# Kernel optimization log

Measured on AMD Instinct MI355X. Metric: run time of the kernel, lower is better.

Reference implementation:

```python
import jax, jax.numpy as jnp
import numpy as np

N_NODES = 100000
N_EDGES = 3200000
IN_CH = 128
HID = 64
N_GRAPHS = 512


def _gcn_conv(x, W, b, src, dst, n_nodes):
    """PyG GCNConv: out = D^{-1/2} (A + I) D^{-1/2} X W + b.
    src/dst are edge endpoints; self-loops handled analytically."""
    h = x @ W  # [N, out]
    # degree with self-loops (count at target nodes, as in PyG)
    deg = jnp.zeros((n_nodes,), h.dtype).at[dst].add(1.0) + 1.0
    dis = jax.lax.rsqrt(deg)  # deg^{-1/2}
    norm = dis[src] * dis[dst]  # [E]
    msg = h[src] * norm[:, None]  # gather + scale, [E, out]
    out = jnp.zeros_like(h).at[dst].add(msg)  # scatter-add
    # self-loop term: norm_ii = 1/deg_i
    out = out + h * (dis * dis)[:, None]
    return out + b


def setup_inputs() -> dict:
    key = jax.random.key(0)
    ks = jax.random.split(key, 8)
    x = jax.random.normal(ks[0], (N_NODES, IN_CH), dtype=jnp.float32)
    edge_index = jax.random.randint(ks[1], (2, N_EDGES), 0, N_NODES, dtype=jnp.int64)
    batch = jnp.sort(jax.random.randint(ks[2], (N_NODES,), 0, N_GRAPHS, dtype=jnp.int64))
    s1 = 1.0 / np.sqrt(IN_CH)
    s2 = 1.0 / np.sqrt(HID)
    W1 = jax.random.uniform(ks[3], (IN_CH, HID), jnp.float32, -s1, s1)
    b1 = jax.random.uniform(ks[4], (HID,), jnp.float32, -s1, s1)
    W2 = jax.random.uniform(ks[5], (HID, HID), jnp.float32, -s2, s2)
    b2 = jax.random.uniform(ks[6], (HID,), jnp.float32, -s2, s2)
    return {"x": x, "edge_index": edge_index, "batch": batch,
            "W1": W1, "b1": b1, "W2": W2, "b2": b2}


def reference(x, edge_index, batch, W1, b1, W2, b2):
    src, dst = edge_index[0], edge_index[1]
    n = x.shape[0]
    h = jax.nn.relu(_gcn_conv(x, W1, b1, src, dst, n))
    h = jax.nn.relu(_gcn_conv(h, W2, b2, src, dst, n))
    # F.dropout(p=0.2) treated as identity (eval / deterministic reference)
    # global_mean_pool: segment mean over graph ids
    sums = jax.ops.segment_sum(h, batch, num_segments=N_GRAPHS)
    cnts = jax.ops.segment_sum(jnp.ones((n,), h.dtype), batch, num_segments=N_GRAPHS)
    return sums / jnp.maximum(cnts, 1.0)[:, None]
```

## Files before the change

kernel.cpp:

```cpp
#include <hip/hip_runtime.h>

typedef unsigned int uint;
typedef unsigned short ushort;
typedef float f32x2 __attribute__((ext_vector_type(2)));

#define N_NODES 100000
#define N_EDGES 3200000
#define IN_CH 128
#define HID 64
#define N_GRAPHS 512
#define EPB 4096
#define NBLK ((N_EDGES + EPB - 1) / EPB)
#define NB 391
#define CAP 10240

__device__ __forceinline__ uint f2bf1(float f) {
    union { float f; uint i; } v; v.f = f;
    return (v.i + 0x7fffu + ((v.i >> 16) & 1u)) >> 16;
}
__device__ __forceinline__ uint pack2(float lo, float hi) {
    return f2bf1(lo) | (f2bf1(hi) << 16);
}
__device__ __forceinline__ float2 ub2(uint u) {
    union { uint i; float f; } a, b;
    a.i = u << 16; b.i = u & 0xffff0000u;
    return make_float2(a.f, b.f);
}
__device__ __forceinline__ f32x2 up2(uint u) {
    union { uint i; float f; } lo, hi;
    lo.i = u << 16; hi.i = u & 0xffff0000u;
    f32x2 r; r.x = lo.f; r.y = hi.f;
    return r;
}

__global__ __launch_bounds__(256) void scatter_kernel(const int* __restrict__ src,
                                                      const int* __restrict__ dst,
                                                      int* __restrict__ bcnt,
                                                      uint* __restrict__ pairs) {
    __shared__ int h4[4 * NB];
    __shared__ int gbase[NB];
    __shared__ int cur[NB];
    __shared__ int scan[512];
    __shared__ uint stage[EPB];
    __shared__ ushort sbid[EPB];
    int t = threadIdx.x;
    int base = blockIdx.x * EPB;

    int rs[16], rd[16];
#pragma unroll
    for (int j = 0; j < 16; ++j) {
        int e = base + j * 256 + t;
        if (e < N_EDGES) { rs[j] = src[e]; rd[j] = dst[e]; }
        else rd[j] = -1;
    }
    for (int i = t; i < 4 * NB; i += 256) h4[i] = 0;
    __syncthreads();
    int w = t >> 6;
#pragma unroll
    for (int j = 0; j < 16; ++j)
        if (rd[j] >= 0) atomicAdd(&h4[w * NB + (rd[j] >> 8)], 1);
    __syncthreads();

    for (int b = t; b < 512; b += 256)
        scan[b] = (b < NB) ? (h4[b] + h4[NB + b] + h4[2 * NB + b] + h4[3 * NB + b]) : 0;
    __syncthreads();
#pragma unroll
    for (int o = 1; o < 512; o <<= 1) {
        int a0 = (t >= o) ? scan[t - o] : 0;
        int a1 = (t + 256 >= o) ? scan[t + 256 - o] : 0;
        __syncthreads();
        scan[t] += a0;
        scan[t + 256] += a1;
        __syncthreads();
    }

    for (int b = t; b < NB; b += 256) {
        int cnt = h4[b] + h4[NB + b] + h4[2 * NB + b] + h4[3 * NB + b];
        int loff = scan[b] - cnt;
        int start = cnt ? atomicAdd(&bcnt[b * 16], cnt) : 0;
        gbase[b] = b * CAP + start - loff;
        cur[b] = loff;
    }
    __syncthreads();

#pragma unroll
    for (int j = 0; j < 16; ++j) {
        if (rd[j] >= 0) {
            int b = rd[j] >> 8;
            int r = atomicAdd(&cur[b], 1);
            stage[r] = ((uint)(rd[j] & 255) << 24) | (uint)rs[j];
            sbid[r] = (ushort)b;
        }
    }
    __syncthreads();

    int total = scan[NB - 1];
    for (int i = t; i < total; i += 256)
        pairs[(size_t)gbase[sbid[i]] + i] = stage[i];
}

__global__ __launch_bounds__(512) void bucket_csr_kernel(const uint* __restrict__ pairs,
                                                         const int* __restrict__ bcnt,
                                                         int* __restrict__ csr_src,
                                                         int* __restrict__ rstart,
                                                         int* __restrict__ rend,
                                                         float* __restrict__ dis) {
    __shared__ int h8[8 * 256];
    __shared__ int h[256];
    int b = blockIdx.x;
    int t = threadIdx.x;
    int w = t >> 6;
    int e0 = b * CAP;
    int e1 = e0 + bcnt[b * 16];

    for (int i = t; i < 8 * 256; i += 512) h8[i] = 0;
    __syncthreads();

    int* hw = &h8[w * 256];
    int e = e0 + t;
    for (; e + 1536 < e1; e += 2048) {
        uint p0 = pairs[e], p1 = pairs[e + 512], p2 = pairs[e + 1024], p3 = pairs[e + 1536];
        atomicAdd(&hw[p0 >> 24], 1);
        atomicAdd(&hw[p1 >> 24], 1);
        atomicAdd(&hw[p2 >> 24], 1);
        atomicAdd(&hw[p3 >> 24], 1);
    }
    for (; e < e1; e += 512)
        atomicAdd(&hw[pairs[e] >> 24], 1);
    __syncthreads();

    int v = 0;
    if (t < 256) {
#pragma unroll
        for (int j = 0; j < 8; ++j) v += h8[j * 256 + t];
        h[t] = v;
    }
    __syncthreads();
#pragma unroll
    for (int o = 1; o < 256; o <<= 1) {
        int x = (t >= o && t < 256) ? h[t - o] : 0;
        __syncthreads();
        if (t < 256) h[t] += x;
        __syncthreads();
    }
    int excl = (t < 256) ? h[t] - v : 0;
    int n = b * 256 + t;
    if (t < 256 && n < N_NODES) {
        rstart[n] = e0 + excl;
        rend[n] = e0 + excl + v;
        dis[n] = rsqrtf((float)v + 1.0f);
    }
    __syncthreads();
    if (t < 256) h[t] = e0 + excl;
    __syncthreads();

    e = e0 + t;
    for (; e + 1536 < e1; e += 2048) {
        uint p0 = pairs[e], p1 = pairs[e + 512], p2 = pairs[e + 1024], p3 = pairs[e + 1536];
        int q0 = atomicAdd(&h[p0 >> 24], 1);
        int q1 = atomicAdd(&h[p1 >> 24], 1);
        int q2 = atomicAdd(&h[p2 >> 24], 1);
        int q3 = atomicAdd(&h[p3 >> 24], 1);
        csr_src[q0] = (int)(p0 & 0xFFFFFFu);
        csr_src[q1] = (int)(p1 & 0xFFFFFFu);
        csr_src[q2] = (int)(p2 & 0xFFFFFFu);
        csr_src[q3] = (int)(p3 & 0xFFFFFFu);
    }
    for (; e < e1; e += 512) {
        uint p = pairs[e];
        int pos = atomicAdd(&h[p >> 24], 1);
        csr_src[pos] = (int)(p & 0xFFFFFFu);
    }
}

__global__ __launch_bounds__(256) void gemm1_kernel(const float* __restrict__ X,
                                                    const float* __restrict__ W,
                                                    const float* __restrict__ dis,
                                                    uint* __restrict__ Y) {
    __shared__ float Wl[IN_CH * 64];
    __shared__ float Xs[128 * 33];
    int t = threadIdx.x;
    for (int idx = t; idx < IN_CH * 64; idx += 256) Wl[idx] = W[idx];

    int r0 = (t >> 3) * 4;
    int c0 = (t & 7) * 8;
    int rowBase = blockIdx.x * 128;

    float acc[4][8];
#pragma unroll
    for (int a = 0; a < 4; ++a)
#pragma unroll
        for (int c = 0; c < 8; ++c) acc[a][c] = 0.f;

    int srow = t >> 1;
    int shh = (t & 1) * 16;
    bool sok = (rowBase + srow) < N_NODES;
    const float* xbase = X + (size_t)(rowBase + srow) * IN_CH + shh;

    float4 nx[4];
#pragma unroll
    for (int f = 0; f < 4; ++f)
        nx[f] = sok ? *reinterpret_cast<const float4*>(xbase + f * 4)
                    : make_float4(0.f, 0.f, 0.f, 0.f);

    for (int kc = 0; kc < IN_CH; kc += 32) {
        if (kc) __syncthreads();
#pragma unroll
        for (int f = 0; f < 4; ++f) {
            int o = srow * 33 + shh + f * 4;
            Xs[o] = nx[f].x; Xs[o + 1] = nx[f].y; Xs[o + 2] = nx[f].z; Xs[o + 3] = nx[f].w;
        }
        __syncthreads();
        if (kc + 32 < IN_CH) {
#pragma unroll
            for (int f = 0; f < 4; ++f)
                nx[f] = sok ? *reinterpret_cast<const float4*>(xbase + kc + 32 + f * 4)
                            : make_float4(0.f, 0.f, 0.f, 0.f);
        }
#pragma unroll
        for (int kk = 0; kk < 32; ++kk) {
            const float4 wa = *reinterpret_cast<const float4*>(&Wl[(kc + kk) * 64 + c0]);
            const float4 wb = *reinterpret_cast<const float4*>(&Wl[(kc + kk) * 64 + c0 + 4]);
            float xr[4];
#pragma unroll
            for (int a = 0; a < 4; ++a) xr[a] = Xs[(r0 + a) * 33 + kk];
#pragma unroll
            for (int a = 0; a < 4; ++a) {
                acc[a][0] += xr[a] * wa.x; acc[a][1] += xr[a] * wa.y;
                acc[a][2] += xr[a] * wa.z; acc[a][3] += xr[a] * wa.w;
                acc[a][4] += xr[a] * wb.x; acc[a][5] += xr[a] * wb.y;
                acc[a][6] += xr[a] * wb.z; acc[a][7] += xr[a] * wb.w;
            }
        }
    }
#pragma unroll
    for (int a = 0; a < 4; ++a) {
        int row = rowBase + r0 + a;
        if (row < N_NODES) {
            float d = dis[row];
            uint4 o;
            o.x = pack2(acc[a][0] * d, acc[a][1] * d);
            o.y = pack2(acc[a][2] * d, acc[a][3] * d);
            o.z = pack2(acc[a][4] * d, acc[a][5] * d);
            o.w = pack2(acc[a][6] * d, acc[a][7] * d);
            *reinterpret_cast<uint4*>(Y + (size_t)row * 32 + (t & 7) * 4) = o;
        }
    }
}

__global__ __launch_bounds__(256) void gemm2_kernel(const uint* __restrict__ X,
                                                    const float* __restrict__ W,
                                                    const float* __restrict__ dis,
                                                    uint* __restrict__ Y) {
    __shared__ float Wl[HID * 64];
    __shared__ float Xs[128 * 33];
    int t = threadIdx.x;
    for (int idx = t; idx < HID * 64; idx += 256) Wl[idx] = W[idx];

    int r0 = (t >> 3) * 4;
    int c0 = (t & 7) * 8;
    int rowBase = blockIdx.x * 128;

    float acc[4][8];
#pragma unroll
    for (int a = 0; a < 4; ++a)
#pragma unroll
        for (int c = 0; c < 8; ++c) acc[a][c] = 0.f;

    int srow = t >> 1;
    int shh = (t & 1) * 16;
    bool sok = (rowBase + srow) < N_NODES;
    const uint* xbase = X + (size_t)(rowBase + srow) * 32 + (t & 1) * 8;

    uint4 n0_ = make_uint4(0, 0, 0, 0), n1_ = n0_;
    if (sok) {
        n0_ = *reinterpret_cast<const uint4*>(xbase);
        n1_ = *reinterpret_cast<const uint4*>(xbase + 4);
    }

    for (int kc = 0; kc < HID; kc += 32) {
        if (kc) __syncthreads();
        {
            uint us[8] = {n0_.x, n0_.y, n0_.z, n0_.w, n1_.x, n1_.y, n1_.z, n1_.w};
            int o = srow * 33 + shh;
#pragma unroll
            for (int j = 0; j < 8; ++j) {
                float2 f = ub2(us[j]);
                Xs[o + 2 * j]     = fmaxf(f.x, 0.f);
                Xs[o + 2 * j + 1] = fmaxf(f.y, 0.f);
            }
        }
        __syncthreads();
        if (kc + 32 < HID && sok) {
            n0_ = *reinterpret_cast<const uint4*>(xbase + 16);
            n1_ = *reinterpret_cast<const uint4*>(xbase + 20);
        }
#pragma unroll
        for (int kk = 0; kk < 32; ++kk) {
            const float4 wa = *reinterpret_cast<const float4*>(&Wl[(kc + kk) * 64 + c0]);
            const float4 wb = *reinterpret_cast<const float4*>(&Wl[(kc + kk) * 64 + c0 + 4]);
            float xr[4];
#pragma unroll
            for (int a = 0; a < 4; ++a) xr[a] = Xs[(r0 + a) * 33 + kk];
#pragma unroll
            for (int a = 0; a < 4; ++a) {
                acc[a][0] += xr[a] * wa.x; acc[a][1] += xr[a] * wa.y;
                acc[a][2] += xr[a] * wa.z; acc[a][3] += xr[a] * wa.w;
                acc[a][4] += xr[a] * wb.x; acc[a][5] += xr[a] * wb.y;
                acc[a][6] += xr[a] * wb.z; acc[a][7] += xr[a] * wb.w;
            }
        }
    }
#pragma unroll
    for (int a = 0; a < 4; ++a) {
        int row = rowBase + r0 + a;
        if (row < N_NODES) {
            float d = dis[row];
            uint4 o;
            o.x = pack2(acc[a][0] * d, acc[a][1] * d);
            o.y = pack2(acc[a][2] * d, acc[a][3] * d);
            o.z = pack2(acc[a][4] * d, acc[a][5] * d);
            o.w = pack2(acc[a][6] * d, acc[a][7] * d);
            *reinterpret_cast<uint4*>(Y + (size_t)row * 32 + (t & 7) * 4) = o;
        }
    }
}

__global__ __launch_bounds__(256) void gather_kernel(const int* __restrict__ rstart,
                                                     const int* __restrict__ rend,
                                                     const int* __restrict__ csr_src,
                                                     const float* __restrict__ dis,
                                                     const float* __restrict__ bias,
                                                     const uint* __restrict__ A,
                                                     uint* __restrict__ B) {
    int i = blockIdx.x * 4 + (threadIdx.x >> 6);
    if (i >= N_NODES) return;
    int lane = threadIdx.x & 63;
    int q = lane >> 3;
    int cu = (lane & 7) * 4;

    float4 bi0 = *reinterpret_cast<const float4*>(&bias[(lane & 7) * 8]);
    float4 bi1 = *reinterpret_cast<const float4*>(&bias[(lane & 7) * 8 + 4]);

    int e = rstart[i];
    int end = rend[i];

    f32x2 a[4], b[4];
#pragma unroll
    for (int j = 0; j < 4; ++j) { a[j] = (f32x2)0.f; b[j] = (f32x2)0.f; }

    if (q == 0) {
        uint4 u = *reinterpret_cast<const uint4*>(&A[(size_t)i * 32 + cu]);
        a[0] += up2(u.x); a[1] += up2(u.y); a[2] += up2(u.z); a[3] += up2(u.w);
    }
    for (; e + 16 <= end; e += 16) {
        int s0 = csr_src[e + q];
        int s1 = csr_src[e + 8 + q];
        uint4 u0 = *reinterpret_cast<const uint4*>(&A[(size_t)s0 * 32 + cu]);
        uint4 u1 = *reinterpret_cast<const uint4*>(&A[(size_t)s1 * 32 + cu]);
        a[0] += up2(u0.x); a[1] += up2(u0.y); a[2] += up2(u0.z); a[3] += up2(u0.w);
        b[0] += up2(u1.x); b[1] += up2(u1.y); b[2] += up2(u1.z); b[3] += up2(u1.w);
    }
    for (; e + 8 <= end; e += 8) {
        int s = csr_src[e + q];
        uint4 u = *reinterpret_cast<const uint4*>(&A[(size_t)s * 32 + cu]);
        a[0] += up2(u.x); a[1] += up2(u.y); a[2] += up2(u.z); a[3] += up2(u.w);
    }
    if (e + q < end) {
        int s = csr_src[e + q];
        uint4 u = *reinterpret_cast<const uint4*>(&A[(size_t)s * 32 + cu]);
        b[0] += up2(u.x); b[1] += up2(u.y); b[2] += up2(u.z); b[3] += up2(u.w);
    }
    float r[8];
#pragma unroll
    for (int j = 0; j < 4; ++j) {
        f32x2 s = a[j] + b[j];
        r[2 * j] = s.x; r[2 * j + 1] = s.y;
    }
#pragma unroll
    for (int j = 0; j < 8; ++j) {
        r[j] += __shfl_xor(r[j], 8);
        r[j] += __shfl_xor(r[j], 16);
        r[j] += __shfl_xor(r[j], 32);
    }
    if (q == 0) {
        float d = dis[i];
        uint4 o;
        o.x = pack2(bi0.x + d * r[0], bi0.y + d * r[1]);
        o.y = pack2(bi0.z + d * r[2], bi0.w + d * r[3]);
        o.z = pack2(bi1.x + d * r[4], bi1.y + d * r[5]);
        o.w = pack2(bi1.z + d * r[6], bi1.w + d * r[7]);
        *reinterpret_cast<uint4*>(B + (size_t)i * 32 + (lane & 7) * 4) = o;
    }
}

__global__ __launch_bounds__(256) void pool_kernel(const uint* __restrict__ B,
                                                   const int* __restrict__ batch,
                                                   float* __restrict__ sums,
                                                   float* __restrict__ cnt) {
    int w = blockIdx.x * 4 + (threadIdx.x >> 6);
    int half = (threadIdx.x >> 5) & 1;
    int l = threadIdx.x & 31;
    int n0 = w * 32 + half * 16;
    if (n0 >= N_NODES) return;
    int n1 = min(n0 + 16, N_NODES);
    int curg = batch[n0];
    float a0 = 0.f, a1 = 0.f;
    int run = 0;
    for (int n = n0; n < n1; ++n) {
        int g = batch[n];
        if (g != curg) {
            atomicAdd(&sums[curg * 64 + 2 * l], a0);
            atomicAdd(&sums[curg * 64 + 2 * l + 1], a1);
            if (l == 0) atomicAdd(&cnt[curg], (float)run);
            curg = g; a0 = 0.f; a1 = 0.f; run = 0;
        }
        float2 f = ub2(B[(size_t)n * 32 + l]);
        a0 += fmaxf(f.x, 0.f);
        a1 += fmaxf(f.y, 0.f);
        run++;
    }
    atomicAdd(&sums[curg * 64 + 2 * l], a0);
    atomicAdd(&sums[curg * 64 + 2 * l + 1], a1);
    if (l == 0) atomicAdd(&cnt[curg], (float)run);
}

__global__ __launch_bounds__(256) void final_kernel(const float* __restrict__ sums,
                                                    const float* __restrict__ cnt,
                                                    float* __restrict__ out) {
    int idx = blockIdx.x * 256 + threadIdx.x;
    if (idx < N_GRAPHS * 64) out[idx] = sums[idx] / fmaxf(cnt[idx >> 6], 1.0f);
}

extern "C" void kernel_launch(void* const* d_in, const int* in_sizes, int n_in,
                              void* d_out, int out_size, void* d_ws, size_t ws_size,
                              hipStream_t stream) {
    const float* x     = (const float*)d_in[0];
    const int*   edge  = (const int*)d_in[1];
    const int*   batch = (const int*)d_in[2];
    const float* W1    = (const float*)d_in[3];
    const float* b1    = (const float*)d_in[4];
    const float* W2    = (const float*)d_in[5];
    const float* b2    = (const float*)d_in[6];
    float* out = (float*)d_out;

    uint*  A        = (uint*)d_ws;
    uint*  B        = A + (size_t)N_NODES * 32;
    uint*  pairs    = B + (size_t)N_NODES * 32;
    int*   csr_src  = (int*)(pairs + (size_t)NB * CAP);
    float* dis      = (float*)(csr_src + (size_t)NB * CAP);
    int*   rstart   = (int*)(dis + N_NODES);
    int*   rend     = rstart + N_NODES;
    float* sums     = (float*)(rend + N_NODES);
    float* cnt_f    = sums + (size_t)N_GRAPHS * 64;
    int*   bcnt     = (int*)(cnt_f + N_GRAPHS);

    const int* src = edge;
    const int* dst = edge + N_EDGES;

    hipMemsetAsync(sums, 0, (N_GRAPHS * 64 + N_GRAPHS + NB * 16) * sizeof(float), stream);

    scatter_kernel<<<NBLK, 256, 0, stream>>>(src, dst, bcnt, pairs);
    bucket_csr_kernel<<<NB, 512, 0, stream>>>(pairs, bcnt, csr_src, rstart, rend, dis);

    gemm1_kernel<<<(N_NODES + 127) / 128, 256, 0, stream>>>(x, W1, dis, A);
    gather_kernel<<<(N_NODES + 3) / 4, 256, 0, stream>>>(rstart, rend, csr_src, dis, b1, A, B);

    gemm2_kernel<<<(N_NODES + 127) / 128, 256, 0, stream>>>(B, W2, dis, A);
    gather_kernel<<<(N_NODES + 3) / 4, 256, 0, stream>>>(rstart, rend, csr_src, dis, b2, A, B);

    pool_kernel<<<(N_NODES + 127) / 128, 256, 0, stream>>>(B, batch, sums, cnt_f);
    final_kernel<<<(N_GRAPHS * 64 + 255) / 256, 256, 0, stream>>>(sums, cnt_f, out);
}
```

Baseline: 348.8 us.

## Split CSR bucket build across two blocks per bucket and cache pairs in registers

Each destination bucket of 256 nodes is now handled by two blocks, each owning 128 nodes, which doubles the grid size of the CSR-build kernel. Each block loads the bucket's packed pairs into registers once, up to 20 per thread, and reuses them for both the histogram pass and the placement pass instead of reading global memory twice. The upper-half block derives its base offset from the bucket total minus its own count. Every block still reads the whole bucket, so global reads double overall. The fixed register count assumes each bucket holds at most 10240 edges, which relies on CAP being large enough.

```diff
diff --git a/kernel.cpp b/kernel.cpp
--- a/kernel.cpp
+++ b/kernel.cpp
@@ -13,6 +13,7 @@
 #define NBLK ((N_EDGES + EPB - 1) / EPB)
 #define NB 391
 #define CAP 10240
+#define CSR_REGS 20
 
 __device__ __forceinline__ uint f2bf1(float f) {
     union { float f; uint i; } v; v.f = f;
@@ -105,71 +106,78 @@
                                                          int* __restrict__ rstart,
                                                          int* __restrict__ rend,
                                                          float* __restrict__ dis) {
-    __shared__ int h8[8 * 256];
-    __shared__ int h[256];
-    int b = blockIdx.x;
+    __shared__ int h8[8 * 128];
+    __shared__ int h[128];
+    __shared__ int tot_s;
+    int bb = blockIdx.x;
+    int b = bb >> 1;
+    int half = bb & 1;
     int t = threadIdx.x;
     int w = t >> 6;
     int e0 = b * CAP;
-    int e1 = e0 + bcnt[b * 16];
-
-    for (int i = t; i < 8 * 256; i += 512) h8[i] = 0;
-    __syncthreads();
-
-    int* hw = &h8[w * 256];
-    int e = e0 + t;
-    for (; e + 1536 < e1; e += 2048) {
-        uint p0 = pairs[e], p1 = pairs[e + 512], p2 = pairs[e + 1024], p3 = pairs[e + 1536];
-        atomicAdd(&hw[p0 >> 24], 1);
-        atomicAdd(&hw[p1 >> 24], 1);
-        atomicAdd(&hw[p2 >> 24], 1);
-        atomicAdd(&hw[p3 >> 24], 1);
-    }
-    for (; e < e1; e += 512)
-        atomicAdd(&hw[pairs[e] >> 24], 1);
+    int cntb = bcnt[b * 16];
+    int e1 = e0 + cntb;
+
+    for (int i = t; i < 8 * 128; i += 512) h8[i] = 0;
+    if (t == 0) tot_s = 0;
+    __syncthreads();
+
+    uint rp[CSR_REGS];
+#pragma unroll
+    for (int j = 0; j < CSR_REGS; ++j) {
+        int e = e0 + j * 512 + t;
+        rp[j] = (e < e1) ? pairs[e] : 0xFF000000u;
+    }
+
+    int* hw = &h8[w * 128];
+#pragma unroll
+    for (int j = 0; j < CSR_REGS; ++j) {
+        int e = e0 + j * 512 + t;
+        if (e < e1) {
+            int ld = (int)(rp[j] >> 24);
+            if ((ld >> 7) == half) atomicAdd(&hw[ld & 127], 1);
+        }
+    }
     __syncthreads();
 
     int v = 0;
-    if (t < 256) {
-#pragma unroll
-        for (int j = 0; j < 8; ++j) v += h8[j * 256 + t];
+    if (t < 128) {
+#pragma unroll
+        for (int j = 0; j < 8; ++j) v += h8[j * 128 + t];
         h[t] = v;
-    }
-    __syncthreads();
-#pragma unroll
-    for (int o = 1; o < 256; o <<= 1) {
-        int x = (t >= o && t < 256) ? h[t - o] : 0;
-        __syncthreads();
-        if (t < 256) h[t] += x;
-        __syncthreads();
-    }
-    int excl = (t < 256) ? h[t] - v : 0;
-    int n = b * 256 + t;
-    if (t < 256 && n < N_NODES) {
-        rstart[n] = e0 + excl;
-        rend[n] = e0 + excl + v;
+        atomicAdd(&tot_s, v);
+    }
+    __syncthreads();
+#pragma unroll
+    for (int o = 1; o < 128; o <<= 1) {
+        int x = (t >= o && t < 128) ? h[t - o] : 0;
+        __syncthreads();
+        if (t < 128) h[t] += x;
+        __syncthreads();
+    }
+    int base = e0 + (half ? (cntb - tot_s) : 0);
+    int excl = (t < 128) ? h[t] - v : 0;
+    int n = b * 256 + half * 128 + t;
+    if (t < 128 && n < N_NODES) {
+        rstart[n] = base + excl;
+        rend[n] = base + excl + v;
         dis[n] = rsqrtf((float)v + 1.0f);
     }
     __syncthreads();
-    if (t < 256) h[t] = e0 + excl;
-    __syncthreads();
-
-    e = e0 + t;
-    for (; e + 1536 < e1; e += 2048) {
-        uint p0 = pairs[e], p1 = pairs[e + 512], p2 = pairs[e + 1024], p3 = pairs[e + 1536];
-        int q0 = atomicAdd(&h[p0 >> 24], 1);
-        int q1 = atomicAdd(&h[p1 >> 24], 1);
-        int q2 = atomicAdd(&h[p2 >> 24], 1);
-        int q3 = atomicAdd(&h[p3 >> 24], 1);
-        csr_src[q0] = (int)(p0 & 0xFFFFFFu);
-        csr_src[q1] = (int)(p1 & 0xFFFFFFu);
-        csr_src[q2] = (int)(p2 & 0xFFFFFFu);
-        csr_src[q3] = (int)(p3 & 0xFFFFFFu);
-    }
-    for (; e < e1; e += 512) {
-        uint p = pairs[e];
-        int pos = atomicAdd(&h[p >> 24], 1);
-        csr_src[pos] = (int)(p & 0xFFFFFFu);
+    if (t < 128) h[t] = base + excl;
+    __syncthreads();
+
+#pragma unroll
+    for (int j = 0; j < CSR_REGS; ++j) {
+        int e = e0 + j * 512 + t;
+        if (e < e1) {
+            uint p = rp[j];
+            int ld = (int)(p >> 24);
+            if ((ld >> 7) == half) {
+                int pos = atomicAdd(&h[ld & 127], 1);
+                csr_src[pos] = (int)(p & 0xFFFFFFu);
+            }
+        }
     }
 }
 
@@ -461,7 +469,7 @@
     hipMemsetAsync(sums, 0, (N_GRAPHS * 64 + N_GRAPHS + NB * 16) * sizeof(float), stream);
 
     scatter_kernel<<<NBLK, 256, 0, stream>>>(src, dst, bcnt, pairs);
-    bucket_csr_kernel<<<NB, 512, 0, stream>>>(pairs, bcnt, csr_src, rstart, rend, dis);
+    bucket_csr_kernel<<<2 * NB, 512, 0, stream>>>(pairs, bcnt, csr_src, rstart, rend, dis);
 
     gemm1_kernel<<<(N_NODES + 127) / 128, 256, 0, stream>>>(x, W1, dis, A);
     gather_kernel<<<(N_NODES + 3) / 4, 256, 0, stream>>>(rstart, rend, csr_src, dis, b1, A, B);
```

Result: no change. 351.8 us (+0.9%).

## Fuse layer-1 gather with layer-2 GEMM in a single kernel

Applied to the files above, without the earlier changes.

Replaces the separate layer-1 gather and gemm2 kernels with one kernel that aggregates neighbor rows per node, applies bias and ReLU into shared memory, then multiplies by W2 and scales by the degree factor. This removes one launch and the round trip of the intermediate hidden activations through global memory. In exchange, every 4-node block reloads the full W2 matrix into shared memory, and the per-node matvec has lower arithmetic reuse than the tiled GEMM.

```diff
diff --git a/kernel.cpp b/kernel.cpp
--- a/kernel.cpp
+++ b/kernel.cpp
@@ -248,81 +248,95 @@
     }
 }
 
-__global__ __launch_bounds__(256) void gemm2_kernel(const uint* __restrict__ X,
-                                                    const float* __restrict__ W,
-                                                    const float* __restrict__ dis,
-                                                    uint* __restrict__ Y) {
+__global__ __launch_bounds__(256) void gather_gemm2_kernel(const int* __restrict__ rstart,
+                                                           const int* __restrict__ rend,
+                                                           const int* __restrict__ csr_src,
+                                                           const float* __restrict__ dis,
+                                                           const float* __restrict__ bias,
+                                                           const float* __restrict__ W2,
+                                                           const uint* __restrict__ A,
+                                                           uint* __restrict__ Y) {
     __shared__ float Wl[HID * 64];
-    __shared__ float Xs[128 * 33];
+    __shared__ float Brow[4][HID];
     int t = threadIdx.x;
-    for (int idx = t; idx < HID * 64; idx += 256) Wl[idx] = W[idx];
-
-    int r0 = (t >> 3) * 4;
-    int c0 = (t & 7) * 8;
-    int rowBase = blockIdx.x * 128;
-
-    float acc[4][8];
-#pragma unroll
-    for (int a = 0; a < 4; ++a)
-#pragma unroll
-        for (int c = 0; c < 8; ++c) acc[a][c] = 0.f;
-
-    int srow = t >> 1;
-    int shh = (t & 1) * 16;
-    bool sok = (rowBase + srow) < N_NODES;
-    const uint* xbase = X + (size_t)(rowBase + srow) * 32 + (t & 1) * 8;
-
-    uint4 n0_ = make_uint4(0, 0, 0, 0), n1_ = n0_;
-    if (sok) {
-        n0_ = *reinterpret_cast<const uint4*>(xbase);
-        n1_ = *reinterpret_cast<const uint4*>(xbase + 4);
-    }
-
-    for (int kc = 0; kc < HID; kc += 32) {
-        if (kc) __syncthreads();
-        {
-            uint us[8] = {n0_.x, n0_.y, n0_.z, n0_.w, n1_.x, n1_.y, n1_.z, n1_.w};
-            int o = srow * 33 + shh;
-#pragma unroll
-            for (int j = 0; j < 8; ++j) {
-                float2 f = ub2(us[j]);
-                Xs[o + 2 * j]     = fmaxf(f.x, 0.f);
-                Xs[o + 2 * j + 1] = fmaxf(f.y, 0.f);
-            }
-        }
-        __syncthreads();
-        if (kc + 32 < HID && sok) {
-            n0_ = *reinterpret_cast<const uint4*>(xbase + 16);
-            n1_ = *reinterpret_cast<const uint4*>(xbase + 20);
-        }
-#pragma unroll
-        for (int kk = 0; kk < 32; ++kk) {
-            const float4 wa = *reinterpret_cast<const float4*>(&Wl[(kc + kk) * 64 + c0]);
-            const float4 wb = *reinterpret_cast<const float4*>(&Wl[(kc + kk) * 64 + c0 + 4]);
-            float xr[4];
-#pragma unroll
-            for (int a = 0; a < 4; ++a) xr[a] = Xs[(r0 + a) * 33 + kk];
-#pragma unroll
-            for (int a = 0; a < 4; ++a) {
-                acc[a][0] += xr[a] * wa.x; acc[a][1] += xr[a] * wa.y;
-                acc[a][2] += xr[a] * wa.z; acc[a][3] += xr[a] * wa.w;
-                acc[a][4] += xr[a] * wb.x; acc[a][5] += xr[a] * wb.y;
-                acc[a][6] += xr[a] * wb.z; acc[a][7] += xr[a] * wb.w;
-            }
-        }
-    }
-#pragma unroll
-    for (int a = 0; a < 4; ++a) {
-        int row = rowBase + r0 + a;
-        if (row < N_NODES) {
-            float d = dis[row];
-            uint4 o;
-            o.x = pack2(acc[a][0] * d, acc[a][1] * d);
-            o.y = pack2(acc[a][2] * d, acc[a][3] * d);
-            o.z = pack2(acc[a][4] * d, acc[a][5] * d);
-            o.w = pack2(acc[a][6] * d, acc[a][7] * d);
-            *reinterpret_cast<uint4*>(Y + (size_t)row * 32 + (t & 7) * 4) = o;
-        }
+    for (int idx = t; idx < HID * 64; idx += 256) Wl[idx] = W2[idx];
+
+    int wv = t >> 6;
+    int i = blockIdx.x * 4 + wv;
+    int lane = t & 63;
+    int q = lane >> 3;
+    int cu = (lane & 7) * 4;
+    bool ok = i < N_NODES;
+    float d = ok ? dis[i] : 0.f;
+
+    if (ok) {
+        float4 bi0 = *reinterpret_cast<const float4*>(&bias[(lane & 7) * 8]);
+        float4 bi1 = *reinterpret_cast<const float4*>(&bias[(lane & 7) * 8 + 4]);
+
+        int e = rstart[i];
+        int end = rend[i];
+
+        f32x2 a[4], b[4];
+#pragma unroll
+        for (int j = 0; j < 4; ++j) { a[j] = (f32x2)0.f; b[j] = (f32x2)0.f; }
+
+        if (q == 0) {
+            uint4 u = *reinterpret_cast<const uint4*>(&A[(size_t)i * 32 + cu]);
+            a[0] += up2(u.x); a[1] += up2(u.y); a[2] += up2(u.z); a[3] += up2(u.w);
+        }
+        for (; e + 16 <= end; e += 16) {
+            int s0 = csr_src[e + q];
+            int s1 = csr_src[e + 8 + q];
+            uint4 u0 = *reinterpret_cast<const uint4*>(&A[(size_t)s0 * 32 + cu]);
+            uint4 u1 = *reinterpret_cast<const uint4*>(&A[(size_t)s1 * 32 + cu]);
+            a[0] += up2(u0.x); a[1] += up2(u0.y); a[2] += up2(u0.z); a[3] += up2(u0.w);
+            b[0] += up2(u1.x); b[1] += up2(u1.y); b[2] += up2(u1.z); b[3] += up2(u1.w);
+        }
+        for (; e + 8 <= end; e += 8) {
+            int s = csr_src[e + q];
+            uint4 u = *reinterpret_cast<const uint4*>(&A[(size_t)s * 32 + cu]);
+            a[0] += up2(u.x); a[1] += up2(u.y); a[2] += up2(u.z); a[3] += up2(u.w);
+        }
+        if (e + q < end) {
+            int s = csr_src[e + q];
+            uint4 u = *reinterpret_cast<const uint4*>(&A[(size_t)s * 32 + cu]);
+            b[0] += up2(u.x); b[1] += up2(u.y); b[2] += up2(u.z); b[3] += up2(u.w);
+        }
+        float r[8];
+#pragma unroll
+        for (int j = 0; j < 4; ++j) {
+            f32x2 s = a[j] + b[j];
+            r[2 * j] = s.x; r[2 * j + 1] = s.y;
+        }
+#pragma unroll
+        for (int j = 0; j < 8; ++j) {
+            r[j] += __shfl_xor(r[j], 8);
+            r[j] += __shfl_xor(r[j], 16);
+            r[j] += __shfl_xor(r[j], 32);
+        }
+        if (q == 0) {
+            float* br = &Brow[wv][(lane & 7) * 8];
+            br[0] = fmaxf(bi0.x + d * r[0], 0.f);
+            br[1] = fmaxf(bi0.y + d * r[1], 0.f);
+            br[2] = fmaxf(bi0.z + d * r[2], 0.f);
+            br[3] = fmaxf(bi0.w + d * r[3], 0.f);
+            br[4] = fmaxf(bi1.x + d * r[4], 0.f);
+            br[5] = fmaxf(bi1.y + d * r[5], 0.f);
+            br[6] = fmaxf(bi1.z + d * r[6], 0.f);
+            br[7] = fmaxf(bi1.w + d * r[7], 0.f);
+        }
+    }
+    __syncthreads();
+    if (ok) {
+        const float* br = Brow[wv];
+        float acc = 0.f;
+#pragma unroll
+        for (int k = 0; k < HID; k += 4) {
+            float4 bv = *reinterpret_cast<const float4*>(&br[k]);
+            acc += bv.x * Wl[k * 64 + lane] + bv.y * Wl[(k + 1) * 64 + lane]
+                 + bv.z * Wl[(k + 2) * 64 + lane] + bv.w * Wl[(k + 3) * 64 + lane];
+        }
+        ((ushort*)Y)[(size_t)i * 64 + lane] = (ushort)f2bf1(acc * d);
     }
 }
 
@@ -464,11 +478,12 @@
     bucket_csr_kernel<<<NB, 512, 0, stream>>>(pairs, bcnt, csr_src, rstart, rend, dis);
 
     gemm1_kernel<<<(N_NODES + 127) / 128, 256, 0, stream>>>(x, W1, dis, A);
-    gather_kernel<<<(N_NODES + 3) / 4, 256, 0, stream>>>(rstart, rend, csr_src, dis, b1, A, B);
-
-    gemm2_kernel<<<(N_NODES + 127) / 128, 256, 0, stream>>>(B, W2, dis, A);
-    gather_kernel<<<(N_NODES + 3) / 4, 256, 0, stream>>>(rstart, rend, csr_src, dis, b2, A, B);
-
-    pool_kernel<<<(N_NODES + 127) / 128, 256, 0, stream>>>(B, batch, sums, cnt_f);
+
+    gather_gemm2_kernel<<<(N_NODES + 3) / 4, 256, 0, stream>>>(
+        rstart, rend, csr_src, dis, b1, W2, A, B);
+
+    gather_kernel<<<(N_NODES + 3) / 4, 256, 0, stream>>>(rstart, rend, csr_src, dis, b2, B, A);
+
+    pool_kernel<<<(N_NODES + 127) / 128, 256, 0, stream>>>(A, batch, sums, cnt_f);
     final_kernel<<<(N_GRAPHS * 64 + 255) / 256, 256, 0, stream>>>(sums, cnt_f, out);
 }
```

Measured after the change: 370.2 us. 1.06x slower.
